# Kernel tuning notes

Measured on AMD Instinct MI355X. Metric: run time of the kernel, lower is better.

The kernel has to match this reference:

```python
import jax, jax.numpy as jnp
import numpy as np

B, LQ, LK = 4, 512, 512
QS, KS, H, DV = 512, 512, 256, 512


def setup_inputs() -> dict:
    key = jax.random.key(0)
    ks = jax.random.split(key, 9)
    s_q = 1.0 / np.sqrt(QS)
    s_k = 1.0 / np.sqrt(KS)
    s_v = 1.0 / np.sqrt(H)
    return {
        "query": jax.random.normal(ks[0], (B, LQ, QS), jnp.float32),
        "key": jax.random.normal(ks[1], (B, LK, KS), jnp.float32),
        "value": jax.random.normal(ks[2], (B, LK, DV), jnp.float32),
        "wq": jax.random.uniform(ks[3], (H, QS), jnp.float32, -s_q, s_q),
        "bq": jax.random.uniform(ks[4], (H,), jnp.float32, -s_q, s_q),
        "wk": jax.random.uniform(ks[5], (H, KS), jnp.float32, -s_k, s_k),
        "bk": jax.random.uniform(ks[6], (H,), jnp.float32, -s_k, s_k),
        "wv": jax.random.uniform(ks[7], (H,), jnp.float32, -s_v, s_v),
        "bv": jax.random.uniform(ks[8], (), jnp.float32, -s_v, s_v),
    }


def reference(query, key, value, wq, bq, wk, bk, wv, bv):
    # q: [B, Lq, H], k: [B, Lk, H]
    q = jnp.einsum('bqd,hd->bqh', query, wq) + bq
    k = jnp.einsum('bkd,hd->bkh', key, wk) + bk
    # broadcast add -> [B, Lq, Lk, H], tanh, project to scalar score
    feats = jnp.tanh(q[:, :, None, :] + k[:, None, :, :])
    scores = jnp.einsum('bqkh,h->bqk', feats, wv) + bv  # [B, Lq, Lk]
    attn = jax.nn.softmax(scores, axis=-1)
    # dropout p=0.0 (identity at inference)
    return jnp.einsum('bqk,bkd->bqd', attn, value)
```

## Files before the change

### kernel.cpp

```cpp
#include <hip/hip_runtime.h>

#define LOG2E 1.4426950408889634f

constexpr int Bb = 4, LQ = 512, LK = 512, QS = 512, H = 256, DV = 512;
constexpr int M = 2048;

constexpr size_t OFF_EQT = 0;
constexpr size_t OFF_EKT = 2u << 20;
constexpr size_t OFF_PQ  = 4u << 20;
constexpr size_t OFF_ROW = 6u << 20;

using bf16x8 = __attribute__((ext_vector_type(8))) short;
using f32x4v = __attribute__((ext_vector_type(4))) float;

__device__ inline unsigned short f2bf(float x) {
    unsigned int u = __float_as_uint(x);
    u += 0x7FFFu + ((u >> 16) & 1u);
    return (unsigned short)(u >> 16);
}
__device__ inline unsigned int pk2(float lo, float hi) {
    return (unsigned int)f2bf(lo) | ((unsigned int)f2bf(hi) << 16);
}

__global__ __launch_bounds__(256) void proj_mfma(
    const float* __restrict__ query, const float* __restrict__ key,
    const float* __restrict__ wq, const float* __restrict__ wk,
    const float* __restrict__ bq, const float* __restrict__ bk,
    char* __restrict__ ws, float scale)
{
    const int z = blockIdx.z;
    const float* A    = z ? key : query;
    const float* W    = z ? wk : wq;
    const float* bias = z ? bk : bq;
    float* out = (float*)(ws + (z ? OFF_EKT : OFF_EQT));

    __shared__ unsigned short Als[64][136];
    __shared__ unsigned short Wls[64][136];
    __shared__ float Ot[64][68];

    const int mb = blockIdx.x * 64, nb = blockIdx.y * 64;
    const int tid = threadIdx.x;
    const int wid = tid >> 6, lane = tid & 63;
    const int ml = lane & 15, quad = lane >> 4;

    f32x4v acc[4] = {{0,0,0,0},{0,0,0,0},{0,0,0,0},{0,0,0,0}};

    for (int kc = 0; kc < QS; kc += 128) {
        __syncthreads();
#pragma unroll
        for (int it = 0; it < 4; ++it) {
            int u = tid + it * 256;
            int row = u >> 4, c8 = (u & 15) * 8;
            float4 a0 = *(const float4*)(A + (size_t)(mb + row) * 512 + kc + c8);
            float4 a1 = *(const float4*)(A + (size_t)(mb + row) * 512 + kc + c8 + 4);
            uint4 pa = { pk2(a0.x, a0.y), pk2(a0.z, a0.w), pk2(a1.x, a1.y), pk2(a1.z, a1.w) };
            *(uint4*)&Als[row][c8] = pa;
            float4 w0 = *(const float4*)(W + (size_t)(nb + row) * 512 + kc + c8);
            float4 w1 = *(const float4*)(W + (size_t)(nb + row) * 512 + kc + c8 + 4);
            uint4 pw = { pk2(w0.x, w0.y), pk2(w0.z, w0.w), pk2(w1.x, w1.y), pk2(w1.z, w1.w) };
            *(uint4*)&Wls[row][c8] = pw;
        }
        __syncthreads();
#pragma unroll
        for (int s = 0; s < 4; ++s) {
            int k = s * 32 + quad * 8;
            bf16x8 af = *(const bf16x8*)&Als[wid * 16 + ml][k];
#pragma unroll
            for (int nt = 0; nt < 4; ++nt) {
                bf16x8 bfr = *(const bf16x8*)&Wls[nt * 16 + ml][k];
                acc[nt] = __builtin_amdgcn_mfma_f32_16x16x32_bf16(af, bfr, acc[nt], 0, 0, 0);
            }
        }
    }
    __syncthreads();
#pragma unroll
    for (int nt = 0; nt < 4; ++nt)
#pragma unroll
        for (int r = 0; r < 4; ++r)
            Ot[nt * 16 + ml][wid * 16 + quad * 4 + r] = acc[nt][r];
    __syncthreads();
    {
        int r0 = tid >> 2;
        int c0 = (tid & 3) * 16;
        float bs = bias[nb + r0];
#pragma unroll
        for (int g = 0; g < 4; ++g) {
            float4 v = *(const float4*)&Ot[r0][c0 + g * 4];
            float4 o;
            o.x = __builtin_amdgcn_exp2f(fminf(fmaxf(scale * (v.x + bs), -15.f), 15.f));
            o.y = __builtin_amdgcn_exp2f(fminf(fmaxf(scale * (v.y + bs), -15.f), 15.f));
            o.z = __builtin_amdgcn_exp2f(fminf(fmaxf(scale * (v.z + bs), -15.f), 15.f));
            o.w = __builtin_amdgcn_exp2f(fminf(fmaxf(scale * (v.w + bs), -15.f), 15.f));
            *(float4*)(out + (size_t)(nb + r0) * 2048 + mb + c0 + g * 4) = o;
        }
    }
}

__global__ __launch_bounds__(256, 1) void score_kernel(
    const float* __restrict__ wvp, char* __restrict__ ws)
{
    const float* EqT = (const float*)(ws + OFF_EQT);
    const float* EkT = (const float*)(ws + OFF_EKT);
    unsigned short* Pq = (unsigned short*)(ws + OFF_PQ);
    float* rowpart = (float*)(ws + OFF_ROW);

    __shared__ float Qs[64][64];
    __shared__ float Ks[64][64];
    __shared__ float Wv2[H];
    __shared__ float redS[4][64];

    const int b  = blockIdx.z;
    const int qb = blockIdx.x * 64;
    const int kt = blockIdx.y;
    const int kb = kt * 64;
    const int tid = threadIdx.x;
    const int tx = tid & 15;
    const int ty = tid >> 4;
    const int w  = tid >> 6;
    const int lane = tid & 63;

    Wv2[tid] = wvp[tid] * (2.0f * LOG2E);

    const int mq = b * LQ + qb;
    const int mk = b * LK + kb;
    const int sh = tid >> 4;
    const int sm = (tid & 15) * 4;

    float acc[4][4] = {};

    for (int h0 = 0; h0 < H; h0 += 64) {
        __syncthreads();
#pragma unroll
        for (int it = 0; it < 4; ++it) {
            int h = sh + 16 * it;
            *(float4*)&Qs[h][sm] = *(const float4*)(EqT + (size_t)(h0 + h) * M + mq + sm);
            *(float4*)&Ks[h][sm] = *(const float4*)(EkT + (size_t)(h0 + h) * M + mk + sm);
        }
        __syncthreads();
#pragma unroll 4
        for (int hh = 0; hh < 64; hh += 4) {
            float4 q1 = *(const float4*)&Qs[hh][tx * 4];
            float4 q2 = *(const float4*)&Qs[hh + 1][tx * 4];
            float4 q3 = *(const float4*)&Qs[hh + 2][tx * 4];
            float4 q4 = *(const float4*)&Qs[hh + 3][tx * 4];
            float4 k1 = *(const float4*)&Ks[hh][ty * 4];
            float4 k2 = *(const float4*)&Ks[hh + 1][ty * 4];
            float4 k3 = *(const float4*)&Ks[hh + 2][ty * 4];
            float4 k4 = *(const float4*)&Ks[hh + 3][ty * 4];
            float4 w4v = *(const float4*)&Wv2[h0 + hh];
            const float w1 = w4v.x, w2 = w4v.y, w3 = w4v.z, w4 = w4v.w;
            const float q1a[4] = {q1.x, q1.y, q1.z, q1.w};
            const float q2a[4] = {q2.x, q2.y, q2.z, q2.w};
            const float q3a[4] = {q3.x, q3.y, q3.z, q3.w};
            const float q4a[4] = {q4.x, q4.y, q4.z, q4.w};
            const float k1a[4] = {k1.x, k1.y, k1.z, k1.w};
            const float k2a[4] = {k2.x, k2.y, k2.z, k2.w};
            const float k3a[4] = {k3.x, k3.y, k3.z, k3.w};
            const float k4a[4] = {k4.x, k4.y, k4.z, k4.w};
#pragma unroll
            for (int i = 0; i < 4; ++i)
#pragma unroll
                for (int j = 0; j < 4; ++j) {
                    float ta = fmaf(q1a[i], k1a[j], 1.0f);
                    float tb = fmaf(q2a[i], k2a[j], 1.0f);
                    float tc = fmaf(q3a[i], k3a[j], 1.0f);
                    float td = fmaf(q4a[i], k4a[j], 1.0f);
                    float t12 = ta * tb;
                    float t34 = tc * td;
                    float n12 = fmaf(w1, tb, w2 * ta);
                    float n34 = fmaf(w3, td, w4 * tc);
                    float num = fmaf(n12, t34, n34 * t12);
                    float den = t12 * t34;
                    acc[i][j] = fmaf(num, __builtin_amdgcn_rcpf(den), acc[i][j]);
                }
        }
    }

    float ps[4];
#pragma unroll
    for (int i = 0; i < 4; ++i) {
        int q = qb + tx * 4 + i;
        float p0 = __builtin_amdgcn_exp2f(-acc[i][0]);
        float p1 = __builtin_amdgcn_exp2f(-acc[i][1]);
        float p2 = __builtin_amdgcn_exp2f(-acc[i][2]);
        float p3 = __builtin_amdgcn_exp2f(-acc[i][3]);
        ps[i] = (p0 + p1) + (p2 + p3);
        uint2 o = { pk2(p0, p1), pk2(p2, p3) };
        *(uint2*)(Pq + ((size_t)(b * 512 + q) * 512 + kb + ty * 4)) = o;
    }
#pragma unroll
    for (int i = 0; i < 4; ++i) {
        ps[i] += __shfl_xor(ps[i], 16, 64);
        ps[i] += __shfl_xor(ps[i], 32, 64);
    }
    if (lane < 16) {
#pragma unroll
        for (int i = 0; i < 4; ++i) redS[w][tx * 4 + i] = ps[i];
    }
    __syncthreads();
    if (tid < 64) {
        float s = (redS[0][tid] + redS[1][tid]) + (redS[2][tid] + redS[3][tid]);
        rowpart[(size_t)kt * 2048 + b * 512 + qb + tid] = s;
    }
}

__global__ __launch_bounds__(256) void av_mfma(
    const float* __restrict__ V, const char* __restrict__ wsc,
    float* __restrict__ O)
{
    const unsigned short* Pq = (const unsigned short*)(wsc + OFF_PQ);
    const float* rowpart = (const float*)(wsc + OFF_ROW);

    __shared__ unsigned short Pls[64][136];
    __shared__ unsigned short Vls[64][136];

    const int b = blockIdx.z, qb = blockIdx.x * 64, nb = blockIdx.y * 64;
    const int tid = threadIdx.x;
    const int wid = tid >> 6, lane = tid & 63;
    const int ml = lane & 15, quad = lane >> 4;
    const unsigned short* Pb = Pq + (size_t)b * 512 * 512;
    const float* Vb = V + (size_t)b * 512 * 512;

    f32x4v acc[4] = {{0,0,0,0},{0,0,0,0},{0,0,0,0},{0,0,0,0}};

    for (int kc = 0; kc < LK; kc += 128) {
        __syncthreads();
#pragma unroll
        for (int it = 0; it < 4; ++it) {
            int u = tid + it * 256;
            int row = u >> 4, c8 = (u & 15) * 8;
            *(uint4*)&Pls[row][c8] = *(const uint4*)(Pb + (size_t)(qb + row) * 512 + kc + c8);
        }
#pragma unroll
        for (int it = 0; it < 8; ++it) {
            int u = tid + it * 256;
            int k = u >> 4, c4 = (u & 15) * 4;
            float4 v4 = *(const float4*)(Vb + (size_t)(kc + k) * 512 + nb + c4);
            Vls[c4 + 0][k] = f2bf(v4.x);
            Vls[c4 + 1][k] = f2bf(v4.y);
            Vls[c4 + 2][k] = f2bf(v4.z);
            Vls[c4 + 3][k] = f2bf(v4.w);
        }
        __syncthreads();
#pragma unroll
        for (int s = 0; s < 4; ++s) {
            int k = s * 32 + quad * 8;
            bf16x8 af = *(const bf16x8*)&Pls[wid * 16 + ml][k];
#pragma unroll
            for (int nt = 0; nt < 4; ++nt) {
                bf16x8 bfr = *(const bf16x8*)&Vls[nt * 16 + ml][k];
                acc[nt] = __builtin_amdgcn_mfma_f32_16x16x32_bf16(af, bfr, acc[nt], 0, 0, 0);
            }
        }
    }

    float rr[4];
#pragma unroll
    for (int r = 0; r < 4; ++r) {
        int q = qb + wid * 16 + quad * 4 + r;
        float rs = 0.f;
#pragma unroll
        for (int t = 0; t < 8; ++t) rs += rowpart[(size_t)t * 2048 + b * 512 + q];
        rr[r] = 1.0f / rs;
    }
#pragma unroll
    for (int nt = 0; nt < 4; ++nt)
#pragma unroll
        for (int r = 0; r < 4; ++r) {
            int q = qb + wid * 16 + quad * 4 + r;
            O[((size_t)b * 512 + q) * 512 + nb + nt * 16 + ml] = acc[nt][r] * rr[r];
        }
}

extern "C" void kernel_launch(void* const* d_in, const int* in_sizes, int n_in,
                              void* d_out, int out_size, void* d_ws, size_t ws_size,
                              hipStream_t stream) {
    const float* query = (const float*)d_in[0];
    const float* key   = (const float*)d_in[1];
    const float* value = (const float*)d_in[2];
    const float* wq    = (const float*)d_in[3];
    const float* bq    = (const float*)d_in[4];
    const float* wk    = (const float*)d_in[5];
    const float* bk    = (const float*)d_in[6];
    const float* wv    = (const float*)d_in[7];
    float* out = (float*)d_out;
    char* ws = (char*)d_ws;

    const float c2 = 2.0f * LOG2E;

    proj_mfma<<<dim3(32, 4, 2), 256, 0, stream>>>(query, key, wq, wk, bq, bk, ws, c2);
    score_kernel<<<dim3(8, 8, Bb), 256, 0, stream>>>(wv, ws);
    av_mfma<<<dim3(8, 8, Bb), 256, 0, stream>>>(value, ws, out);
}
```

Baseline: 138.8 us.

## Fuse three kernels into one cooperative kernel with grid syncs

Merges the projection, score and AV kernels into a single cooperative launch of 256 blocks, separated by grid-wide barriers, with one shared-memory arena reused across phases. The aim is to remove two kernel launch gaps and inter-kernel drain/fill overhead. In exchange it adds cooperative launch overhead and grid.sync cost. Each phase is fixed at 256 blocks with launch bounds set to one block per CU, which may limit latency hiding in the projection and AV phases.

```diff
diff --git a/kernel.cpp b/kernel.cpp
--- a/kernel.cpp
+++ b/kernel.cpp
@@ -1,4 +1,7 @@
 #include <hip/hip_runtime.h>
+#include <hip/hip_cooperative_groups.h>
+
+namespace cg = cooperative_groups;
 
 #define LOG2E 1.4426950408889634f
 
@@ -22,254 +25,262 @@
     return (unsigned int)f2bf(lo) | ((unsigned int)f2bf(hi) << 16);
 }
 
-__global__ __launch_bounds__(256) void proj_mfma(
+__global__ __launch_bounds__(256, 1) void fused_kernel(
     const float* __restrict__ query, const float* __restrict__ key,
+    const float* __restrict__ value,
     const float* __restrict__ wq, const float* __restrict__ wk,
     const float* __restrict__ bq, const float* __restrict__ bk,
-    char* __restrict__ ws, float scale)
+    const float* __restrict__ wvp,
+    char* __restrict__ ws, float* __restrict__ out_, float scale)
 {
-    const int z = blockIdx.z;
-    const float* A    = z ? key : query;
-    const float* W    = z ? wk : wq;
-    const float* bias = z ? bk : bq;
-    float* out = (float*)(ws + (z ? OFF_EKT : OFF_EQT));
-
-    __shared__ unsigned short Als[64][136];
-    __shared__ unsigned short Wls[64][136];
-    __shared__ float Ot[64][68];
-
-    const int mb = blockIdx.x * 64, nb = blockIdx.y * 64;
+    cg::grid_group grid = cg::this_grid();
+
+    __shared__ __align__(16) char arena[52224];
+
     const int tid = threadIdx.x;
+    const int bid = blockIdx.x;
     const int wid = tid >> 6, lane = tid & 63;
     const int ml = lane & 15, quad = lane >> 4;
 
-    f32x4v acc[4] = {{0,0,0,0},{0,0,0,0},{0,0,0,0},{0,0,0,0}};
-
-    for (int kc = 0; kc < QS; kc += 128) {
+    {
+        auto Als = (unsigned short (*)[136])(arena);
+        auto Wls = (unsigned short (*)[136])(arena + 17408);
+        auto Ot  = (float (*)[68])(arena + 34816);
+
+        const int z   = bid >> 7;
+        const int rem = bid & 127;
+        const int mb  = (rem >> 2) * 64;
+        const int nb  = (rem & 3) * 64;
+        const float* A    = z ? key : query;
+        const float* W    = z ? wk : wq;
+        const float* bias = z ? bk : bq;
+        float* outp = (float*)(ws + (z ? OFF_EKT : OFF_EQT));
+
+        f32x4v acc[4] = {{0,0,0,0},{0,0,0,0},{0,0,0,0},{0,0,0,0}};
+
+        for (int kc = 0; kc < QS; kc += 128) {
+            __syncthreads();
+#pragma unroll
+            for (int it = 0; it < 4; ++it) {
+                int u = tid + it * 256;
+                int row = u >> 4, c8 = (u & 15) * 8;
+                float4 a0 = *(const float4*)(A + (size_t)(mb + row) * 512 + kc + c8);
+                float4 a1 = *(const float4*)(A + (size_t)(mb + row) * 512 + kc + c8 + 4);
+                uint4 pa = { pk2(a0.x, a0.y), pk2(a0.z, a0.w), pk2(a1.x, a1.y), pk2(a1.z, a1.w) };
+                *(uint4*)&Als[row][c8] = pa;
+                float4 w0 = *(const float4*)(W + (size_t)(nb + row) * 512 + kc + c8);
+                float4 w1 = *(const float4*)(W + (size_t)(nb + row) * 512 + kc + c8 + 4);
+                uint4 pw = { pk2(w0.x, w0.y), pk2(w0.z, w0.w), pk2(w1.x, w1.y), pk2(w1.z, w1.w) };
+                *(uint4*)&Wls[row][c8] = pw;
+            }
+            __syncthreads();
+#pragma unroll
+            for (int s = 0; s < 4; ++s) {
+                int k = s * 32 + quad * 8;
+                bf16x8 af = *(const bf16x8*)&Als[wid * 16 + ml][k];
+#pragma unroll
+                for (int nt = 0; nt < 4; ++nt) {
+                    bf16x8 bfr = *(const bf16x8*)&Wls[nt * 16 + ml][k];
+                    acc[nt] = __builtin_amdgcn_mfma_f32_16x16x32_bf16(af, bfr, acc[nt], 0, 0, 0);
+                }
+            }
+        }
         __syncthreads();
 #pragma unroll
-        for (int it = 0; it < 4; ++it) {
-            int u = tid + it * 256;
-            int row = u >> 4, c8 = (u & 15) * 8;
-            float4 a0 = *(const float4*)(A + (size_t)(mb + row) * 512 + kc + c8);
-            float4 a1 = *(const float4*)(A + (size_t)(mb + row) * 512 + kc + c8 + 4);
-            uint4 pa = { pk2(a0.x, a0.y), pk2(a0.z, a0.w), pk2(a1.x, a1.y), pk2(a1.z, a1.w) };
-            *(uint4*)&Als[row][c8] = pa;
-            float4 w0 = *(const float4*)(W + (size_t)(nb + row) * 512 + kc + c8);
-            float4 w1 = *(const float4*)(W + (size_t)(nb + row) * 512 + kc + c8 + 4);
-            uint4 pw = { pk2(w0.x, w0.y), pk2(w0.z, w0.w), pk2(w1.x, w1.y), pk2(w1.z, w1.w) };
-            *(uint4*)&Wls[row][c8] = pw;
-        }
+        for (int nt = 0; nt < 4; ++nt)
+#pragma unroll
+            for (int r = 0; r < 4; ++r)
+                Ot[nt * 16 + ml][wid * 16 + quad * 4 + r] = acc[nt][r];
         __syncthreads();
-#pragma unroll
-        for (int s = 0; s < 4; ++s) {
-            int k = s * 32 + quad * 8;
-            bf16x8 af = *(const bf16x8*)&Als[wid * 16 + ml][k];
-#pragma unroll
-            for (int nt = 0; nt < 4; ++nt) {
-                bf16x8 bfr = *(const bf16x8*)&Wls[nt * 16 + ml][k];
-                acc[nt] = __builtin_amdgcn_mfma_f32_16x16x32_bf16(af, bfr, acc[nt], 0, 0, 0);
+        {
+            int r0 = tid >> 2;
+            int c0 = (tid & 3) * 16;
+            float bs = bias[nb + r0];
+#pragma unroll
+            for (int g = 0; g < 4; ++g) {
+                float4 v = *(const float4*)&Ot[r0][c0 + g * 4];
+                float4 o;
+                o.x = __builtin_amdgcn_exp2f(fminf(fmaxf(scale * (v.x + bs), -15.f), 15.f));
+                o.y = __builtin_amdgcn_exp2f(fminf(fmaxf(scale * (v.y + bs), -15.f), 15.f));
+                o.z = __builtin_amdgcn_exp2f(fminf(fmaxf(scale * (v.z + bs), -15.f), 15.f));
+                o.w = __builtin_amdgcn_exp2f(fminf(fmaxf(scale * (v.w + bs), -15.f), 15.f));
+                *(float4*)(outp + (size_t)(nb + r0) * 2048 + mb + c0 + g * 4) = o;
             }
         }
     }
-    __syncthreads();
-#pragma unroll
-    for (int nt = 0; nt < 4; ++nt)
-#pragma unroll
-        for (int r = 0; r < 4; ++r)
-            Ot[nt * 16 + ml][wid * 16 + quad * 4 + r] = acc[nt][r];
-    __syncthreads();
+
+    grid.sync();
+
     {
-        int r0 = tid >> 2;
-        int c0 = (tid & 3) * 16;
-        float bs = bias[nb + r0];
-#pragma unroll
-        for (int g = 0; g < 4; ++g) {
-            float4 v = *(const float4*)&Ot[r0][c0 + g * 4];
-            float4 o;
-            o.x = __builtin_amdgcn_exp2f(fminf(fmaxf(scale * (v.x + bs), -15.f), 15.f));
-            o.y = __builtin_amdgcn_exp2f(fminf(fmaxf(scale * (v.y + bs), -15.f), 15.f));
-            o.z = __builtin_amdgcn_exp2f(fminf(fmaxf(scale * (v.z + bs), -15.f), 15.f));
-            o.w = __builtin_amdgcn_exp2f(fminf(fmaxf(scale * (v.w + bs), -15.f), 15.f));
-            *(float4*)(out + (size_t)(nb + r0) * 2048 + mb + c0 + g * 4) = o;
+        const float* EqT = (const float*)(ws + OFF_EQT);
+        const float* EkT = (const float*)(ws + OFF_EKT);
+        unsigned short* Pq = (unsigned short*)(ws + OFF_PQ);
+        float* rowpart = (float*)(ws + OFF_ROW);
+
+        auto Qs   = (float (*)[64])(arena);
+        auto Ks   = (float (*)[64])(arena + 16384);
+        float* Wv2 = (float*)(arena + 32768);
+        auto redS = (float (*)[64])(arena + 33792);
+
+        const int b   = bid >> 6;
+        const int rem = bid & 63;
+        const int qb  = (rem >> 3) * 64;
+        const int kt  = rem & 7;
+        const int kb  = kt * 64;
+        const int tx = tid & 15;
+        const int ty = tid >> 4;
+
+        Wv2[tid] = wvp[tid] * (2.0f * LOG2E);
+
+        const int mq = b * LQ + qb;
+        const int mk = b * LK + kb;
+        const int sh = tid >> 4;
+        const int sm = (tid & 15) * 4;
+
+        float acc[4][4] = {};
+
+        for (int h0 = 0; h0 < H; h0 += 64) {
+            __syncthreads();
+#pragma unroll
+            for (int it = 0; it < 4; ++it) {
+                int h = sh + 16 * it;
+                *(float4*)&Qs[h][sm] = *(const float4*)(EqT + (size_t)(h0 + h) * M + mq + sm);
+                *(float4*)&Ks[h][sm] = *(const float4*)(EkT + (size_t)(h0 + h) * M + mk + sm);
+            }
+            __syncthreads();
+#pragma unroll 4
+            for (int hh = 0; hh < 64; hh += 4) {
+                float4 q1 = *(const float4*)&Qs[hh][tx * 4];
+                float4 q2 = *(const float4*)&Qs[hh + 1][tx * 4];
+                float4 q3 = *(const float4*)&Qs[hh + 2][tx * 4];
+                float4 q4 = *(const float4*)&Qs[hh + 3][tx * 4];
+                float4 k1 = *(const float4*)&Ks[hh][ty * 4];
+                float4 k2 = *(const float4*)&Ks[hh + 1][ty * 4];
+                float4 k3 = *(const float4*)&Ks[hh + 2][ty * 4];
+                float4 k4 = *(const float4*)&Ks[hh + 3][ty * 4];
+                float4 w4v = *(const float4*)&Wv2[h0 + hh];
+                const float w1 = w4v.x, w2 = w4v.y, w3 = w4v.z, w4 = w4v.w;
+                const float q1a[4] = {q1.x, q1.y, q1.z, q1.w};
+                const float q2a[4] = {q2.x, q2.y, q2.z, q2.w};
+                const float q3a[4] = {q3.x, q3.y, q3.z, q3.w};
+                const float q4a[4] = {q4.x, q4.y, q4.z, q4.w};
+                const float k1a[4] = {k1.x, k1.y, k1.z, k1.w};
+                const float k2a[4] = {k2.x, k2.y, k2.z, k2.w};
+                const float k3a[4] = {k3.x, k3.y, k3.z, k3.w};
+                const float k4a[4] = {k4.x, k4.y, k4.z, k4.w};
+#pragma unroll
+                for (int i = 0; i < 4; ++i)
+#pragma unroll
+                    for (int j = 0; j < 4; ++j) {
+                        float ta = fmaf(q1a[i], k1a[j], 1.0f);
+                        float tb = fmaf(q2a[i], k2a[j], 1.0f);
+                        float tc = fmaf(q3a[i], k3a[j], 1.0f);
+                        float td = fmaf(q4a[i], k4a[j], 1.0f);
+                        float t12 = ta * tb;
+                        float t34 = tc * td;
+                        float n12 = fmaf(w1, tb, w2 * ta);
+                        float n34 = fmaf(w3, td, w4 * tc);
+                        float num = fmaf(n12, t34, n34 * t12);
+                        float den = t12 * t34;
+                        acc[i][j] = fmaf(num, __builtin_amdgcn_rcpf(den), acc[i][j]);
+                    }
+            }
+        }
+
+        float ps[4];
+#pragma unroll
+        for (int i = 0; i < 4; ++i) {
+            int q = qb + tx * 4 + i;
+            float p0 = __builtin_amdgcn_exp2f(-acc[i][0]);
+            float p1 = __builtin_amdgcn_exp2f(-acc[i][1]);
+            float p2 = __builtin_amdgcn_exp2f(-acc[i][2]);
+            float p3 = __builtin_amdgcn_exp2f(-acc[i][3]);
+            ps[i] = (p0 + p1) + (p2 + p3);
+            uint2 o = { pk2(p0, p1), pk2(p2, p3) };
+            *(uint2*)(Pq + ((size_t)(b * 512 + q) * 512 + kb + ty * 4)) = o;
+        }
+#pragma unroll
+        for (int i = 0; i < 4; ++i) {
+            ps[i] += __shfl_xor(ps[i], 16, 64);
+            ps[i] += __shfl_xor(ps[i], 32, 64);
+        }
+        if (lane < 16) {
+#pragma unroll
+            for (int i = 0; i < 4; ++i) redS[wid][tx * 4 + i] = ps[i];
+        }
+        __syncthreads();
+        if (tid < 64) {
+            float s = (redS[0][tid] + redS[1][tid]) + (redS[2][tid] + redS[3][tid]);
+            rowpart[(size_t)kt * 2048 + b * 512 + qb + tid] = s;
         }
     }
-}
-
-__global__ __launch_bounds__(256, 1) void score_kernel(
-    const float* __restrict__ wvp, char* __restrict__ ws)
-{
-    const float* EqT = (const float*)(ws + OFF_EQT);
-    const float* EkT = (const float*)(ws + OFF_EKT);
-    unsigned short* Pq = (unsigned short*)(ws + OFF_PQ);
-    float* rowpart = (float*)(ws + OFF_ROW);
-
-    __shared__ float Qs[64][64];
-    __shared__ float Ks[64][64];
-    __shared__ float Wv2[H];
-    __shared__ float redS[4][64];
-
-    const int b  = blockIdx.z;
-    const int qb = blockIdx.x * 64;
-    const int kt = blockIdx.y;
-    const int kb = kt * 64;
-    const int tid = threadIdx.x;
-    const int tx = tid & 15;
-    const int ty = tid >> 4;
-    const int w  = tid >> 6;
-    const int lane = tid & 63;
-
-    Wv2[tid] = wvp[tid] * (2.0f * LOG2E);
-
-    const int mq = b * LQ + qb;
-    const int mk = b * LK + kb;
-    const int sh = tid >> 4;
-    const int sm = (tid & 15) * 4;
-
-    float acc[4][4] = {};
-
-    for (int h0 = 0; h0 < H; h0 += 64) {
-        __syncthreads();
-#pragma unroll
-        for (int it = 0; it < 4; ++it) {
-            int h = sh + 16 * it;
-            *(float4*)&Qs[h][sm] = *(const float4*)(EqT + (size_t)(h0 + h) * M + mq + sm);
-            *(float4*)&Ks[h][sm] = *(const float4*)(EkT + (size_t)(h0 + h) * M + mk + sm);
-        }
-        __syncthreads();
-#pragma unroll 4
-        for (int hh = 0; hh < 64; hh += 4) {
-            float4 q1 = *(const float4*)&Qs[hh][tx * 4];
-            float4 q2 = *(const float4*)&Qs[hh + 1][tx * 4];
-            float4 q3 = *(const float4*)&Qs[hh + 2][tx * 4];
-            float4 q4 = *(const float4*)&Qs[hh + 3][tx * 4];
-            float4 k1 = *(const float4*)&Ks[hh][ty * 4];
-            float4 k2 = *(const float4*)&Ks[hh + 1][ty * 4];
-            float4 k3 = *(const float4*)&Ks[hh + 2][ty * 4];
-            float4 k4 = *(const float4*)&Ks[hh + 3][ty * 4];
-            float4 w4v = *(const float4*)&Wv2[h0 + hh];
-            const float w1 = w4v.x, w2 = w4v.y, w3 = w4v.z, w4 = w4v.w;
-            const float q1a[4] = {q1.x, q1.y, q1.z, q1.w};
-            const float q2a[4] = {q2.x, q2.y, q2.z, q2.w};
-            const float q3a[4] = {q3.x, q3.y, q3.z, q3.w};
-            const float q4a[4] = {q4.x, q4.y, q4.z, q4.w};
-            const float k1a[4] = {k1.x, k1.y, k1.z, k1.w};
-            const float k2a[4] = {k2.x, k2.y, k2.z, k2.w};
-            const float k3a[4] = {k3.x, k3.y, k3.z, k3.w};
-            const float k4a[4] = {k4.x, k4.y, k4.z, k4.w};
-#pragma unroll
-            for (int i = 0; i < 4; ++i)
-#pragma unroll
-                for (int j = 0; j < 4; ++j) {
-                    float ta = fmaf(q1a[i], k1a[j], 1.0f);
-                    float tb = fmaf(q2a[i], k2a[j], 1.0f);
-                    float tc = fmaf(q3a[i], k3a[j], 1.0f);
-                    float td = fmaf(q4a[i], k4a[j], 1.0f);
-                    float t12 = ta * tb;
-                    float t34 = tc * td;
-                    float n12 = fmaf(w1, tb, w2 * ta);
-                    float n34 = fmaf(w3, td, w4 * tc);
-                    float num = fmaf(n12, t34, n34 * t12);
-                    float den = t12 * t34;
-                    acc[i][j] = fmaf(num, __builtin_amdgcn_rcpf(den), acc[i][j]);
+
+    grid.sync();
+
+    {
+        const unsigned short* Pq = (const unsigned short*)(ws + OFF_PQ);
+        const float* rowpart = (const float*)(ws + OFF_ROW);
+
+        auto Pls = (unsigned short (*)[136])(arena);
+        auto Vls = (unsigned short (*)[136])(arena + 17408);
+
+        const int b   = bid >> 6;
+        const int rem = bid & 63;
+        const int qb  = (rem >> 3) * 64;
+        const int nb  = (rem & 7) * 64;
+        const unsigned short* Pb = Pq + (size_t)b * 512 * 512;
+        const float* Vb = value + (size_t)b * 512 * 512;
+
+        f32x4v acc[4] = {{0,0,0,0},{0,0,0,0},{0,0,0,0},{0,0,0,0}};
+
+        for (int kc = 0; kc < LK; kc += 128) {
+            __syncthreads();
+#pragma unroll
+            for (int it = 0; it < 4; ++it) {
+                int u = tid + it * 256;
+                int row = u >> 4, c8 = (u & 15) * 8;
+                *(uint4*)&Pls[row][c8] = *(const uint4*)(Pb + (size_t)(qb + row) * 512 + kc + c8);
+            }
+#pragma unroll
+            for (int it = 0; it < 8; ++it) {
+                int u = tid + it * 256;
+                int k = u >> 4, c4 = (u & 15) * 4;
+                float4 v4 = *(const float4*)(Vb + (size_t)(kc + k) * 512 + nb + c4);
+                Vls[c4 + 0][k] = f2bf(v4.x);
+                Vls[c4 + 1][k] = f2bf(v4.y);
+                Vls[c4 + 2][k] = f2bf(v4.z);
+                Vls[c4 + 3][k] = f2bf(v4.w);
+            }
+            __syncthreads();
+#pragma unroll
+            for (int s = 0; s < 4; ++s) {
+                int k = s * 32 + quad * 8;
+                bf16x8 af = *(const bf16x8*)&Pls[wid * 16 + ml][k];
+#pragma unroll
+                for (int nt = 0; nt < 4; ++nt) {
+                    bf16x8 bfr = *(const bf16x8*)&Vls[nt * 16 + ml][k];
+                    acc[nt] = __builtin_amdgcn_mfma_f32_16x16x32_bf16(af, bfr, acc[nt], 0, 0, 0);
                 }
-        }
-    }
-
-    float ps[4];
-#pragma unroll
-    for (int i = 0; i < 4; ++i) {
-        int q = qb + tx * 4 + i;
-        float p0 = __builtin_amdgcn_exp2f(-acc[i][0]);
-        float p1 = __builtin_amdgcn_exp2f(-acc[i][1]);
-        float p2 = __builtin_amdgcn_exp2f(-acc[i][2]);
-        float p3 = __builtin_amdgcn_exp2f(-acc[i][3]);
-        ps[i] = (p0 + p1) + (p2 + p3);
-        uint2 o = { pk2(p0, p1), pk2(p2, p3) };
-        *(uint2*)(Pq + ((size_t)(b * 512 + q) * 512 + kb + ty * 4)) = o;
-    }
-#pragma unroll
-    for (int i = 0; i < 4; ++i) {
-        ps[i] += __shfl_xor(ps[i], 16, 64);
-        ps[i] += __shfl_xor(ps[i], 32, 64);
-    }
-    if (lane < 16) {
-#pragma unroll
-        for (int i = 0; i < 4; ++i) redS[w][tx * 4 + i] = ps[i];
-    }
-    __syncthreads();
-    if (tid < 64) {
-        float s = (redS[0][tid] + redS[1][tid]) + (redS[2][tid] + redS[3][tid]);
-        rowpart[(size_t)kt * 2048 + b * 512 + qb + tid] = s;
-    }
-}
-
-__global__ __launch_bounds__(256) void av_mfma(
-    const float* __restrict__ V, const char* __restrict__ wsc,
-    float* __restrict__ O)
-{
-    const unsigned short* Pq = (const unsigned short*)(wsc + OFF_PQ);
-    const float* rowpart = (const float*)(wsc + OFF_ROW);
-
-    __shared__ unsigned short Pls[64][136];
-    __shared__ unsigned short Vls[64][136];
-
-    const int b = blockIdx.z, qb = blockIdx.x * 64, nb = blockIdx.y * 64;
-    const int tid = threadIdx.x;
-    const int wid = tid >> 6, lane = tid & 63;
-    const int ml = lane & 15, quad = lane >> 4;
-    const unsigned short* Pb = Pq + (size_t)b * 512 * 512;
-    const float* Vb = V + (size_t)b * 512 * 512;
-
-    f32x4v acc[4] = {{0,0,0,0},{0,0,0,0},{0,0,0,0},{0,0,0,0}};
-
-    for (int kc = 0; kc < LK; kc += 128) {
-        __syncthreads();
-#pragma unroll
-        for (int it = 0; it < 4; ++it) {
-            int u = tid + it * 256;
-            int row = u >> 4, c8 = (u & 15) * 8;
-            *(uint4*)&Pls[row][c8] = *(const uint4*)(Pb + (size_t)(qb + row) * 512 + kc + c8);
-        }
-#pragma unroll
-        for (int it = 0; it < 8; ++it) {
-            int u = tid + it * 256;
-            int k = u >> 4, c4 = (u & 15) * 4;
-            float4 v4 = *(const float4*)(Vb + (size_t)(kc + k) * 512 + nb + c4);
-            Vls[c4 + 0][k] = f2bf(v4.x);
-            Vls[c4 + 1][k] = f2bf(v4.y);
-            Vls[c4 + 2][k] = f2bf(v4.z);
-            Vls[c4 + 3][k] = f2bf(v4.w);
-        }
-        __syncthreads();
-#pragma unroll
-        for (int s = 0; s < 4; ++s) {
-            int k = s * 32 + quad * 8;
-            bf16x8 af = *(const bf16x8*)&Pls[wid * 16 + ml][k];
-#pragma unroll
-            for (int nt = 0; nt < 4; ++nt) {
-                bf16x8 bfr = *(const bf16x8*)&Vls[nt * 16 + ml][k];
-                acc[nt] = __builtin_amdgcn_mfma_f32_16x16x32_bf16(af, bfr, acc[nt], 0, 0, 0);
-            }
-        }
-    }
-
-    float rr[4];
-#pragma unroll
-    for (int r = 0; r < 4; ++r) {
-        int q = qb + wid * 16 + quad * 4 + r;
-        float rs = 0.f;
-#pragma unroll
-        for (int t = 0; t < 8; ++t) rs += rowpart[(size_t)t * 2048 + b * 512 + q];
-        rr[r] = 1.0f / rs;
-    }
-#pragma unroll
-    for (int nt = 0; nt < 4; ++nt)
+            }
+        }
+
+        float rr[4];
 #pragma unroll
         for (int r = 0; r < 4; ++r) {
             int q = qb + wid * 16 + quad * 4 + r;
-            O[((size_t)b * 512 + q) * 512 + nb + nt * 16 + ml] = acc[nt][r] * rr[r];
-        }
+            float rs = 0.f;
+#pragma unroll
+            for (int t = 0; t < 8; ++t) rs += rowpart[(size_t)t * 2048 + b * 512 + q];
+            rr[r] = 1.0f / rs;
+        }
+#pragma unroll
+        for (int nt = 0; nt < 4; ++nt)
+#pragma unroll
+            for (int r = 0; r < 4; ++r) {
+                int q = qb + wid * 16 + quad * 4 + r;
+                out_[((size_t)b * 512 + q) * 512 + nb + nt * 16 + ml] = acc[nt][r] * rr[r];
+            }
+    }
 }
 
 extern "C" void kernel_launch(void* const* d_in, const int* in_sizes, int n_in,
@@ -286,9 +297,13 @@
     float* out = (float*)d_out;
     char* ws = (char*)d_ws;
 
-    const float c2 = 2.0f * LOG2E;
-
-    proj_mfma<<<dim3(32, 4, 2), 256, 0, stream>>>(query, key, wq, wk, bq, bk, ws, c2);
-    score_kernel<<<dim3(8, 8, Bb), 256, 0, stream>>>(wv, ws);
-    av_mfma<<<dim3(8, 8, Bb), 256, 0, stream>>>(value, ws, out);
+    float c2 = 2.0f * LOG2E;
+
+    void* args[] = {
+        (void*)&query, (void*)&key, (void*)&value,
+        (void*)&wq, (void*)&wk, (void*)&bq, (void*)&bk, (void*)&wv,
+        (void*)&ws, (void*)&out, (void*)&c2
+    };
+    hipLaunchCooperativeKernel((const void*)fused_kernel,
+                               dim3(256), dim3(256), args, 0, stream);
 }
```

After: 210.6 us. +51.7%, slower.
